# Optimization experiments

Measured on AMD Instinct MI355X. Metric: run time of the kernel, lower is better.

The kernel has to match this reference:

```python
import jax, jax.numpy as jnp
import numpy as np

EPS = 1e-5

def _bn(x, g, b, m, v):
    # inference-mode batchnorm with moving statistics
    return (x - m) * jax.lax.rsqrt(v + EPS) * g + b

def setup_inputs() -> dict:
    key = jax.random.key(0)
    ks = jax.random.split(key, 12)
    t, b, s, hu = 512, 64, 1024, 1024
    d_in = s + hu
    si = jax.random.normal(ks[0], (b, s), dtype=jnp.float32)
    h = jax.random.normal(ks[1], (t, b, hu), dtype=jnp.float32)
    W0 = jax.random.normal(ks[2], (d_in, 10), dtype=jnp.float32) * 0.02
    b0 = jnp.zeros((10,), jnp.float32)
    g0 = jnp.ones((10,), jnp.float32)
    be0 = jnp.zeros((10,), jnp.float32)
    m0 = jax.random.normal(ks[3], (10,), dtype=jnp.float32) * 0.1
    v0 = jax.random.uniform(ks[4], (10,), dtype=jnp.float32) + 0.5
    W1 = jax.random.normal(ks[5], (10, 5), dtype=jnp.float32) * 0.3
    b1 = jnp.zeros((5,), jnp.float32)
    g1 = jnp.ones((5,), jnp.float32)
    be1 = jnp.zeros((5,), jnp.float32)
    m1 = jax.random.normal(ks[6], (5,), dtype=jnp.float32) * 0.1
    v1 = jax.random.uniform(ks[7], (5,), dtype=jnp.float32) + 0.5
    W2 = jax.random.normal(ks[8], (5, 1), dtype=jnp.float32) * 0.4
    b2 = jnp.zeros((1,), jnp.float32)
    return {"si": si, "h": h, "W0": W0, "b0": b0, "g0": g0, "be0": be0,
            "m0": m0, "v0": v0, "W1": W1, "b1": b1, "g1": g1, "be1": be1,
            "m1": m1, "v1": v1, "W2": W2, "b2": b2}

def reference(si, h, W0, b0, g0, be0, m0, v0, W1, b1, g1, be1, m1, v1, W2, b2):
    t, b, hu = h.shape
    # concat decoder state with every encoder hidden state: [t, b, s+hu]
    x = jnp.concatenate([jnp.broadcast_to(si[None], (t,) + si.shape), h], axis=-1)
    x = jax.nn.relu(_bn(x @ W0 + b0, g0, be0, m0, v0))
    x = jax.nn.relu(_bn(x @ W1 + b1, g1, be1, m1, v1))
    scores = x @ W2 + b2                       # [t, b, 1]
    # original: tf.concat over axis 0 -> [t*b, 1], softmax over axis 0 (ALL t*b entries)
    a = jax.nn.softmax(scores.reshape(t * b))  # [t*b]
    # original uses only the first t rows of the flattened softmax as scalar weights
    ci = jnp.einsum('t,tbh->bh', a[:t], h)     # [b, hu]
    return ci
```

## Files before the change

kernel.cpp:

```cpp
#include <hip/hip_runtime.h>

#define EPS 1e-5f

constexpr int T  = 512;
constexpr int B  = 64;
constexpr int HU = 1024;
constexpr int S  = 1024;
constexpr int P  = T * B;
constexpr int C  = B * HU;

constexpr size_t OFF_SIW0   = 0;
constexpr size_t OFF_SCORES = 1024;
constexpr size_t OFF_A      = 34816;
constexpr size_t OFF_PART   = 35840;

__global__ __launch_bounds__(256) void k_siw0(const float* __restrict__ si,
                                              const float* __restrict__ W0,
                                              float* __restrict__ out) {
    const int b   = blockIdx.x;
    const int tid = threadIdx.x;
    const float4 sv = ((const float4*)(si + (size_t)b * S))[tid];
    const float* wp = W0 + (size_t)(4 * tid) * 10;

    float acc[10];
#pragma unroll
    for (int j = 0; j < 10; ++j) acc[j] = 0.f;
#pragma unroll
    for (int d = 0; d < 4; ++d) {
        const float hx = (&sv.x)[d];
#pragma unroll
        for (int j = 0; j < 10; ++j) acc[j] = fmaf(hx, wp[d * 10 + j], acc[j]);
    }
#pragma unroll
    for (int j = 0; j < 10; ++j) {
#pragma unroll
        for (int off = 32; off > 0; off >>= 1)
            acc[j] += __shfl_down(acc[j], off, 64);
    }
    __shared__ float red[4][10];
    const int wv = tid >> 6, ln = tid & 63;
    if (ln == 0) {
#pragma unroll
        for (int j = 0; j < 10; ++j) red[wv][j] = acc[j];
    }
    __syncthreads();
    if (tid < 10)
        out[(size_t)b * 10 + tid] =
            red[0][tid] + red[1][tid] + red[2][tid] + red[3][tid];
}

__global__ __launch_bounds__(256) void k_scores(
    const float* __restrict__ h,  const float* __restrict__ W0,
    const float* __restrict__ siW0,
    const float* __restrict__ b0, const float* __restrict__ g0,
    const float* __restrict__ be0,const float* __restrict__ m0,
    const float* __restrict__ v0,
    const float* __restrict__ W1, const float* __restrict__ b1,
    const float* __restrict__ g1, const float* __restrict__ be1,
    const float* __restrict__ m1, const float* __restrict__ v1,
    const float* __restrict__ W2, const float* __restrict__ b2,
    float* __restrict__ scores) {
    const int g   = blockIdx.x;
    const int tid = threadIdx.x;
    const int wv  = tid >> 6;
    const int ln  = tid & 63;
    const int p   = g * 64 + ln;
    const float* hrow = h + (size_t)p * HU;
    const int k0 = __builtin_amdgcn_readfirstlane(wv * 256);

    float acc[10];
#pragma unroll
    for (int j = 0; j < 10; ++j) acc[j] = 0.f;

#pragma unroll 4
    for (int i = 0; i < 64; ++i) {
        const int k = k0 + 4 * i;
        const float4 hv = *(const float4*)(hrow + k);
        const float* wp = W0 + (size_t)(1024 + k) * 10;
#pragma unroll
        for (int d = 0; d < 4; ++d) {
            const float hx = (&hv.x)[d];
#pragma unroll
            for (int j = 0; j < 10; ++j)
                acc[j] = fmaf(hx, wp[d * 10 + j], acc[j]);
        }
    }

    __shared__ float part[4][64][10];
#pragma unroll
    for (int j = 0; j < 10; ++j) part[wv][ln][j] = acc[j];
    __syncthreads();

    if (wv == 0) {
        float y[10];
#pragma unroll
        for (int j = 0; j < 10; ++j) {
            float u = part[0][ln][j] + part[1][ln][j] + part[2][ln][j] +
                      part[3][ln][j] + siW0[(size_t)ln * 10 + j] + b0[j];
            u = (u - m0[j]) * (1.0f / sqrtf(v0[j] + EPS)) * g0[j] + be0[j];
            y[j] = fmaxf(u, 0.f);
        }
        float z[5];
#pragma unroll
        for (int i = 0; i < 5; ++i) {
            float u = b1[i];
#pragma unroll
            for (int j = 0; j < 10; ++j) u = fmaf(y[j], W1[j * 5 + i], u);
            u = (u - m1[i]) * (1.0f / sqrtf(v1[i] + EPS)) * g1[i] + be1[i];
            z[i] = fmaxf(u, 0.f);
        }
        float sc = b2[0];
#pragma unroll
        for (int i = 0; i < 5; ++i) sc = fmaf(z[i], W2[i], sc);
        scores[p] = sc;
    }
}

__global__ __launch_bounds__(1024) void k_softmax(const float* __restrict__ scores,
                                                  float* __restrict__ a) {
    const int tid = threadIdx.x;
    __shared__ float red[16];
    __shared__ float s_m, s_z;

    float mx = -3.0e38f;
    for (int i = tid; i < P; i += 1024) mx = fmaxf(mx, scores[i]);
#pragma unroll
    for (int off = 32; off > 0; off >>= 1)
        mx = fmaxf(mx, __shfl_down(mx, off, 64));
    if ((tid & 63) == 0) red[tid >> 6] = mx;
    __syncthreads();
    if (tid == 0) {
        float m = red[0];
        for (int i = 1; i < 16; ++i) m = fmaxf(m, red[i]);
        s_m = m;
    }
    __syncthreads();
    const float m = s_m;

    float sum = 0.f;
    for (int i = tid; i < P; i += 1024) sum += expf(scores[i] - m);
#pragma unroll
    for (int off = 32; off > 0; off >>= 1)
        sum += __shfl_down(sum, off, 64);
    if ((tid & 63) == 0) red[tid >> 6] = sum;
    __syncthreads();
    if (tid == 0) {
        float z = 0.f;
        for (int i = 0; i < 16; ++i) z += red[i];
        s_z = z;
    }
    __syncthreads();

    if (tid < T) a[tid] = expf(scores[tid] - m) / s_z;
}

__global__ __launch_bounds__(256) void k_wsum(const float* __restrict__ h,
                                              const float* __restrict__ a,
                                              float* __restrict__ part) {
    const int cb = blockIdx.x & 63;
    const int ts = blockIdx.x >> 6;
    const int c  = cb * 1024 + threadIdx.x * 4;
    const float* hp = h + (size_t)ts * 64 * C + c;
    const float* ap = a + ts * 64;

    float4 acc = {0.f, 0.f, 0.f, 0.f};
    for (int i = 0; i < 64; ++i) {
        const float av = ap[i];
        const float4 hv = *(const float4*)(hp + (size_t)i * C);
        acc.x = fmaf(av, hv.x, acc.x);
        acc.y = fmaf(av, hv.y, acc.y);
        acc.z = fmaf(av, hv.z, acc.z);
        acc.w = fmaf(av, hv.w, acc.w);
    }
    *(float4*)(part + (size_t)ts * C + c) = acc;
}

__global__ __launch_bounds__(256) void k_reduce(const float* __restrict__ part,
                                                float* __restrict__ out) {
    const int c = blockIdx.x * 1024 + threadIdx.x * 4;
    float4 s = {0.f, 0.f, 0.f, 0.f};
#pragma unroll
    for (int ts = 0; ts < 8; ++ts) {
        const float4 v = *(const float4*)(part + (size_t)ts * C + c);
        s.x += v.x; s.y += v.y; s.z += v.z; s.w += v.w;
    }
    *(float4*)(out + c) = s;
}

extern "C" void kernel_launch(void* const* d_in, const int* in_sizes, int n_in,
                              void* d_out, int out_size, void* d_ws, size_t ws_size,
                              hipStream_t stream) {
    const float* si  = (const float*)d_in[0];
    const float* h   = (const float*)d_in[1];
    const float* W0  = (const float*)d_in[2];
    const float* b0  = (const float*)d_in[3];
    const float* g0  = (const float*)d_in[4];
    const float* be0 = (const float*)d_in[5];
    const float* m0  = (const float*)d_in[6];
    const float* v0  = (const float*)d_in[7];
    const float* W1  = (const float*)d_in[8];
    const float* b1  = (const float*)d_in[9];
    const float* g1  = (const float*)d_in[10];
    const float* be1 = (const float*)d_in[11];
    const float* m1  = (const float*)d_in[12];
    const float* v1  = (const float*)d_in[13];
    const float* W2  = (const float*)d_in[14];
    const float* b2  = (const float*)d_in[15];

    float* ws     = (float*)d_ws;
    float* siW0   = ws + OFF_SIW0;
    float* scores = ws + OFF_SCORES;
    float* a      = ws + OFF_A;
    float* part   = ws + OFF_PART;
    float* out    = (float*)d_out;

    hipLaunchKernelGGL(k_siw0,    dim3(64),  dim3(256),  0, stream, si, W0, siW0);
    hipLaunchKernelGGL(k_scores,  dim3(512), dim3(256),  0, stream, h, W0, siW0,
                       b0, g0, be0, m0, v0, W1, b1, g1, be1, m1, v1, W2, b2, scores);
    hipLaunchKernelGGL(k_softmax, dim3(1),   dim3(1024), 0, stream, scores, a);
    hipLaunchKernelGGL(k_wsum,    dim3(512), dim3(256),  0, stream, h, a, part);
    hipLaunchKernelGGL(k_reduce,  dim3(64),  dim3(256),  0, stream, part, out);
}
```

Baseline: 268.2 us.

## Increase parallelism in scores, softmax, and weighted-sum reduction kernels

```diff
diff --git a/kernel.cpp b/kernel.cpp
--- a/kernel.cpp
+++ b/kernel.cpp
@@ -8,6 +8,7 @@
 constexpr int S  = 1024;
 constexpr int P  = T * B;
 constexpr int C  = B * HU;
+constexpr int TSPLIT = 32;
 
 constexpr size_t OFF_SIW0   = 0;
 constexpr size_t OFF_SCORES = 1024;
@@ -49,7 +50,7 @@
             red[0][tid] + red[1][tid] + red[2][tid] + red[3][tid];
 }
 
-__global__ __launch_bounds__(256) void k_scores(
+__global__ __launch_bounds__(512) void k_scores(
     const float* __restrict__ h,  const float* __restrict__ W0,
     const float* __restrict__ siW0,
     const float* __restrict__ b0, const float* __restrict__ g0,
@@ -66,14 +67,14 @@
     const int ln  = tid & 63;
     const int p   = g * 64 + ln;
     const float* hrow = h + (size_t)p * HU;
-    const int k0 = __builtin_amdgcn_readfirstlane(wv * 256);
+    const int k0 = __builtin_amdgcn_readfirstlane(wv * 128);
 
     float acc[10];
 #pragma unroll
     for (int j = 0; j < 10; ++j) acc[j] = 0.f;
 
-#pragma unroll 4
-    for (int i = 0; i < 64; ++i) {
+#pragma unroll 8
+    for (int i = 0; i < 32; ++i) {
         const int k = k0 + 4 * i;
         const float4 hv = *(const float4*)(hrow + k);
         const float* wp = W0 + (size_t)(1024 + k) * 10;
@@ -86,7 +87,7 @@
         }
     }
 
-    __shared__ float part[4][64][10];
+    __shared__ float part[8][64][10];
 #pragma unroll
     for (int j = 0; j < 10; ++j) part[wv][ln][j] = acc[j];
     __syncthreads();
@@ -95,8 +96,9 @@
         float y[10];
 #pragma unroll
         for (int j = 0; j < 10; ++j) {
-            float u = part[0][ln][j] + part[1][ln][j] + part[2][ln][j] +
-                      part[3][ln][j] + siW0[(size_t)ln * 10 + j] + b0[j];
+            float u = siW0[(size_t)ln * 10 + j] + b0[j];
+#pragma unroll
+            for (int w = 0; w < 8; ++w) u += part[w][ln][j];
             u = (u - m0[j]) * (1.0f / sqrtf(v0[j] + EPS)) * g0[j] + be0[j];
             y[j] = fmaxf(u, 0.f);
         }
@@ -122,8 +124,16 @@
     __shared__ float red[16];
     __shared__ float s_m, s_z;
 
+    float4 v[8];
+#pragma unroll
+    for (int q = 0; q < 8; ++q)
+        v[q] = ((const float4*)scores)[tid + 1024 * q];
+
     float mx = -3.0e38f;
-    for (int i = tid; i < P; i += 1024) mx = fmaxf(mx, scores[i]);
+#pragma unroll
+    for (int q = 0; q < 8; ++q) {
+        mx = fmaxf(mx, fmaxf(fmaxf(v[q].x, v[q].y), fmaxf(v[q].z, v[q].w)));
+    }
 #pragma unroll
     for (int off = 32; off > 0; off >>= 1)
         mx = fmaxf(mx, __shfl_down(mx, off, 64));
@@ -138,7 +148,11 @@
     const float m = s_m;
 
     float sum = 0.f;
-    for (int i = tid; i < P; i += 1024) sum += expf(scores[i] - m);
+#pragma unroll
+    for (int q = 0; q < 8; ++q) {
+        sum += expf(v[q].x - m) + expf(v[q].y - m) +
+               expf(v[q].z - m) + expf(v[q].w - m);
+    }
 #pragma unroll
     for (int off = 32; off > 0; off >>= 1)
         sum += __shfl_down(sum, off, 64);
@@ -151,7 +165,15 @@
     }
     __syncthreads();
 
-    if (tid < T) a[tid] = expf(scores[tid] - m) / s_z;
+    if (tid < T / 4) {
+        const float inv = 1.0f / s_z;
+        float4 o;
+        o.x = expf(v[0].x - m) * inv;
+        o.y = expf(v[0].y - m) * inv;
+        o.z = expf(v[0].z - m) * inv;
+        o.w = expf(v[0].w - m) * inv;
+        ((float4*)a)[tid] = o;
+    }
 }
 
 __global__ __launch_bounds__(256) void k_wsum(const float* __restrict__ h,
@@ -160,11 +182,12 @@
     const int cb = blockIdx.x & 63;
     const int ts = blockIdx.x >> 6;
     const int c  = cb * 1024 + threadIdx.x * 4;
-    const float* hp = h + (size_t)ts * 64 * C + c;
-    const float* ap = a + ts * 64;
+    const float* hp = h + (size_t)ts * 16 * C + c;
+    const float* ap = a + ts * 16;
 
     float4 acc = {0.f, 0.f, 0.f, 0.f};
-    for (int i = 0; i < 64; ++i) {
+#pragma unroll
+    for (int i = 0; i < 16; ++i) {
         const float av = ap[i];
         const float4 hv = *(const float4*)(hp + (size_t)i * C);
         acc.x = fmaf(av, hv.x, acc.x);
@@ -175,12 +198,12 @@
     *(float4*)(part + (size_t)ts * C + c) = acc;
 }
 
-__global__ __launch_bounds__(256) void k_reduce(const float* __restrict__ part,
-                                                float* __restrict__ out) {
-    const int c = blockIdx.x * 1024 + threadIdx.x * 4;
+__global__ __launch_bounds__(64) void k_reduce(const float* __restrict__ part,
+                                               float* __restrict__ out) {
+    const int c = blockIdx.x * 256 + threadIdx.x * 4;
     float4 s = {0.f, 0.f, 0.f, 0.f};
-#pragma unroll
-    for (int ts = 0; ts < 8; ++ts) {
+#pragma unroll 8
+    for (int ts = 0; ts < TSPLIT; ++ts) {
         const float4 v = *(const float4*)(part + (size_t)ts * C + c);
         s.x += v.x; s.y += v.y; s.z += v.z; s.w += v.w;
     }
@@ -214,10 +237,10 @@
     float* part   = ws + OFF_PART;
     float* out    = (float*)d_out;
 
-    hipLaunchKernelGGL(k_siw0,    dim3(64),  dim3(256),  0, stream, si, W0, siW0);
-    hipLaunchKernelGGL(k_scores,  dim3(512), dim3(256),  0, stream, h, W0, siW0,
+    hipLaunchKernelGGL(k_siw0,    dim3(64),   dim3(256),  0, stream, si, W0, siW0);
+    hipLaunchKernelGGL(k_scores,  dim3(512),  dim3(512),  0, stream, h, W0, siW0,
                        b0, g0, be0, m0, v0, W1, b1, g1, be1, m1, v1, W2, b2, scores);
-    hipLaunchKernelGGL(k_softmax, dim3(1),   dim3(1024), 0, stream, scores, a);
-    hipLaunchKernelGGL(k_wsum,    dim3(512), dim3(256),  0, stream, h, a, part);
-    hipLaunchKernelGGL(k_reduce,  dim3(64),  dim3(256),  0, stream, part, out);
-}
+    hipLaunchKernelGGL(k_softmax, dim3(1),    dim3(1024), 0, stream, scores, a);
+    hipLaunchKernelGGL(k_wsum,    dim3(2048), dim3(256),  0, stream, h, a, part);
+    hipLaunchKernelGGL(k_reduce,  dim3(256),  dim3(64),   0, stream, part, out);
+}
```

Measured after the change: 262.8 us. 1.02x faster.

## Fuse softmax and si projection into scores kernel, defer normalization to reduce

Applied to the files above, without the earlier changes.

```diff
diff --git a/kernel.cpp b/kernel.cpp
--- a/kernel.cpp
+++ b/kernel.cpp
@@ -8,50 +8,15 @@
 constexpr int S  = 1024;
 constexpr int P  = T * B;
 constexpr int C  = B * HU;
+constexpr int TSPLIT = 32;
 
-constexpr size_t OFF_SIW0   = 0;
-constexpr size_t OFF_SCORES = 1024;
-constexpr size_t OFF_A      = 34816;
-constexpr size_t OFF_PART   = 35840;
+constexpr size_t OFF_W    = 1024;
+constexpr size_t OFF_ZB   = 2048;
+constexpr size_t OFF_PART = 35840;
 
-__global__ __launch_bounds__(256) void k_siw0(const float* __restrict__ si,
-                                              const float* __restrict__ W0,
-                                              float* __restrict__ out) {
-    const int b   = blockIdx.x;
-    const int tid = threadIdx.x;
-    const float4 sv = ((const float4*)(si + (size_t)b * S))[tid];
-    const float* wp = W0 + (size_t)(4 * tid) * 10;
-
-    float acc[10];
-#pragma unroll
-    for (int j = 0; j < 10; ++j) acc[j] = 0.f;
-#pragma unroll
-    for (int d = 0; d < 4; ++d) {
-        const float hx = (&sv.x)[d];
-#pragma unroll
-        for (int j = 0; j < 10; ++j) acc[j] = fmaf(hx, wp[d * 10 + j], acc[j]);
-    }
-#pragma unroll
-    for (int j = 0; j < 10; ++j) {
-#pragma unroll
-        for (int off = 32; off > 0; off >>= 1)
-            acc[j] += __shfl_down(acc[j], off, 64);
-    }
-    __shared__ float red[4][10];
-    const int wv = tid >> 6, ln = tid & 63;
-    if (ln == 0) {
-#pragma unroll
-        for (int j = 0; j < 10; ++j) red[wv][j] = acc[j];
-    }
-    __syncthreads();
-    if (tid < 10)
-        out[(size_t)b * 10 + tid] =
-            red[0][tid] + red[1][tid] + red[2][tid] + red[3][tid];
-}
-
-__global__ __launch_bounds__(256) void k_scores(
-    const float* __restrict__ h,  const float* __restrict__ W0,
-    const float* __restrict__ siW0,
+__global__ __launch_bounds__(512) void k_scores(
+    const float* __restrict__ h,  const float* __restrict__ si,
+    const float* __restrict__ W0,
     const float* __restrict__ b0, const float* __restrict__ g0,
     const float* __restrict__ be0,const float* __restrict__ m0,
     const float* __restrict__ v0,
@@ -59,34 +24,41 @@
     const float* __restrict__ g1, const float* __restrict__ be1,
     const float* __restrict__ m1, const float* __restrict__ v1,
     const float* __restrict__ W2, const float* __restrict__ b2,
-    float* __restrict__ scores) {
+    float* __restrict__ wout, float* __restrict__ Zb) {
     const int g   = blockIdx.x;
     const int tid = threadIdx.x;
     const int wv  = tid >> 6;
     const int ln  = tid & 63;
     const int p   = g * 64 + ln;
-    const float* hrow = h + (size_t)p * HU;
-    const int k0 = __builtin_amdgcn_readfirstlane(wv * 256);
+    const float* hrow = h  + (size_t)p  * HU;
+    const float* srow = si + (size_t)ln * S;
+    const int k0 = __builtin_amdgcn_readfirstlane(wv * 128);
 
     float acc[10];
 #pragma unroll
     for (int j = 0; j < 10; ++j) acc[j] = 0.f;
 
 #pragma unroll 4
-    for (int i = 0; i < 64; ++i) {
+    for (int i = 0; i < 32; ++i) {
         const int k = k0 + 4 * i;
         const float4 hv = *(const float4*)(hrow + k);
-        const float* wp = W0 + (size_t)(1024 + k) * 10;
+        const float4 sv = *(const float4*)(srow + k);
+        const float* wph = W0 + (size_t)(1024 + k) * 10;
+        const float* wps = W0 + (size_t)k * 10;
 #pragma unroll
         for (int d = 0; d < 4; ++d) {
             const float hx = (&hv.x)[d];
+            const float sx = (&sv.x)[d];
 #pragma unroll
             for (int j = 0; j < 10; ++j)
-                acc[j] = fmaf(hx, wp[d * 10 + j], acc[j]);
+                acc[j] = fmaf(hx, wph[d * 10 + j], acc[j]);
+#pragma unroll
+            for (int j = 0; j < 10; ++j)
+                acc[j] = fmaf(sx, wps[d * 10 + j], acc[j]);
         }
     }
 
-    __shared__ float part[4][64][10];
+    __shared__ float part[8][64][10];
 #pragma unroll
     for (int j = 0; j < 10; ++j) part[wv][ln][j] = acc[j];
     __syncthreads();
@@ -95,8 +67,9 @@
         float y[10];
 #pragma unroll
         for (int j = 0; j < 10; ++j) {
-            float u = part[0][ln][j] + part[1][ln][j] + part[2][ln][j] +
-                      part[3][ln][j] + siW0[(size_t)ln * 10 + j] + b0[j];
+            float u = b0[j];
+#pragma unroll
+            for (int w = 0; w < 8; ++w) u += part[w][ln][j];
             u = (u - m0[j]) * (1.0f / sqrtf(v0[j] + EPS)) * g0[j] + be0[j];
             y[j] = fmaxf(u, 0.f);
         }
@@ -112,59 +85,29 @@
         float sc = b2[0];
 #pragma unroll
         for (int i = 0; i < 5; ++i) sc = fmaf(z[i], W2[i], sc);
-        scores[p] = sc;
+
+        const float e = expf(sc);
+        float zsum = e;
+#pragma unroll
+        for (int off = 32; off > 0; off >>= 1)
+            zsum += __shfl_down(zsum, off, 64);
+        if (ln == 0) Zb[g] = zsum;
+        if (g < 8) wout[p] = e;
     }
 }
 
-__global__ __launch_bounds__(1024) void k_softmax(const float* __restrict__ scores,
-                                                  float* __restrict__ a) {
-    const int tid = threadIdx.x;
-    __shared__ float red[16];
-    __shared__ float s_m, s_z;
-
-    float mx = -3.0e38f;
-    for (int i = tid; i < P; i += 1024) mx = fmaxf(mx, scores[i]);
-#pragma unroll
-    for (int off = 32; off > 0; off >>= 1)
-        mx = fmaxf(mx, __shfl_down(mx, off, 64));
-    if ((tid & 63) == 0) red[tid >> 6] = mx;
-    __syncthreads();
-    if (tid == 0) {
-        float m = red[0];
-        for (int i = 1; i < 16; ++i) m = fmaxf(m, red[i]);
-        s_m = m;
-    }
-    __syncthreads();
-    const float m = s_m;
-
-    float sum = 0.f;
-    for (int i = tid; i < P; i += 1024) sum += expf(scores[i] - m);
-#pragma unroll
-    for (int off = 32; off > 0; off >>= 1)
-        sum += __shfl_down(sum, off, 64);
-    if ((tid & 63) == 0) red[tid >> 6] = sum;
-    __syncthreads();
-    if (tid == 0) {
-        float z = 0.f;
-        for (int i = 0; i < 16; ++i) z += red[i];
-        s_z = z;
-    }
-    __syncthreads();
-
-    if (tid < T) a[tid] = expf(scores[tid] - m) / s_z;
-}
-
 __global__ __launch_bounds__(256) void k_wsum(const float* __restrict__ h,
-                                              const float* __restrict__ a,
+                                              const float* __restrict__ w,
                                               float* __restrict__ part) {
     const int cb = blockIdx.x & 63;
     const int ts = blockIdx.x >> 6;
     const int c  = cb * 1024 + threadIdx.x * 4;
-    const float* hp = h + (size_t)ts * 64 * C + c;
-    const float* ap = a + ts * 64;
+    const float* hp = h + (size_t)ts * 16 * C + c;
+    const float* ap = w + ts * 16;
 
     float4 acc = {0.f, 0.f, 0.f, 0.f};
-    for (int i = 0; i < 64; ++i) {
+#pragma unroll
+    for (int i = 0; i < 16; ++i) {
         const float av = ap[i];
         const float4 hv = *(const float4*)(hp + (size_t)i * C);
         acc.x = fmaf(av, hv.x, acc.x);
@@ -175,15 +118,27 @@
     *(float4*)(part + (size_t)ts * C + c) = acc;
 }
 
-__global__ __launch_bounds__(256) void k_reduce(const float* __restrict__ part,
-                                                float* __restrict__ out) {
-    const int c = blockIdx.x * 1024 + threadIdx.x * 4;
+__global__ __launch_bounds__(64) void k_reduce(const float* __restrict__ part,
+                                               const float* __restrict__ Zb,
+                                               float* __restrict__ out) {
+    const int tid = threadIdx.x;
+
+    const float4 z0 = ((const float4*)Zb)[tid * 2];
+    const float4 z1 = ((const float4*)Zb)[tid * 2 + 1];
+    float zs = z0.x + z0.y + z0.z + z0.w + z1.x + z1.y + z1.z + z1.w;
+#pragma unroll
+    for (int off = 32; off > 0; off >>= 1)
+        zs += __shfl_down(zs, off, 64);
+    const float invZ = 1.0f / __shfl(zs, 0, 64);
+
+    const int c = blockIdx.x * 256 + tid * 4;
     float4 s = {0.f, 0.f, 0.f, 0.f};
-#pragma unroll
-    for (int ts = 0; ts < 8; ++ts) {
+#pragma unroll 8
+    for (int ts = 0; ts < TSPLIT; ++ts) {
         const float4 v = *(const float4*)(part + (size_t)ts * C + c);
         s.x += v.x; s.y += v.y; s.z += v.z; s.w += v.w;
     }
+    s.x *= invZ; s.y *= invZ; s.z *= invZ; s.w *= invZ;
     *(float4*)(out + c) = s;
 }
 
@@ -207,17 +162,14 @@
     const float* W2  = (const float*)d_in[14];
     const float* b2  = (const float*)d_in[15];
 
-    float* ws     = (float*)d_ws;
-    float* siW0   = ws + OFF_SIW0;
-    float* scores = ws + OFF_SCORES;
-    float* a      = ws + OFF_A;
-    float* part   = ws + OFF_PART;
-    float* out    = (float*)d_out;
+    float* ws   = (float*)d_ws;
+    float* w    = ws + OFF_W;
+    float* Zb   = ws + OFF_ZB;
+    float* part = ws + OFF_PART;
+    float* out  = (float*)d_out;
 
-    hipLaunchKernelGGL(k_siw0,    dim3(64),  dim3(256),  0, stream, si, W0, siW0);
-    hipLaunchKernelGGL(k_scores,  dim3(512), dim3(256),  0, stream, h, W0, siW0,
-                       b0, g0, be0, m0, v0, W1, b1, g1, be1, m1, v1, W2, b2, scores);
-    hipLaunchKernelGGL(k_softmax, dim3(1),   dim3(1024), 0, stream, scores, a);
-    hipLaunchKernelGGL(k_wsum,    dim3(512), dim3(256),  0, stream, h, a, part);
-    hipLaunchKernelGGL(k_reduce,  dim3(64),  dim3(256),  0, stream, part, out);
+    hipLaunchKernelGGL(k_scores, dim3(512),  dim3(512), 0, stream, h, si, W0,
+                       b0, g0, be0, m0, v0, W1, b1, g1, be1, m1, v1, W2, b2, w, Zb);
+    hipLaunchKernelGGL(k_wsum,   dim3(2048), dim3(256), 0, stream, h, w, part);
+    hipLaunchKernelGGL(k_reduce, dim3(256),  dim3(64),  0, stream, part, Zb, out);
 }
```

After: 273.7 us. 1.02x slower.
